# Kernel optimization log

Measured on AMD Instinct MI355X. Metric: run time of the kernel, lower is better.

Reference implementation:

```python
import jax, jax.numpy as jnp
import numpy as np

B, T, N, H, D = 8, 128, 170, 4, 16
F = H * D  # 64
LN_EPS = 1e-5
MASK_FILL = -(2.0 ** 15) + 1.0  # -32767, matches torch code


def setup_inputs() -> dict:
    key = jax.random.key(0)
    ks = jax.random.split(key, 16)
    s = 0.05
    def w(k):
        return jax.random.normal(k, (F, F), jnp.float32) * s
    def b(k):
        return jax.random.normal(k, (F,), jnp.float32) * s
    return {
        "x": jax.random.normal(ks[0], (B, T, N, F), jnp.float32),
        "te": jax.random.normal(ks[1], (B, T, N, F), jnp.float32),
        "Wq": w(ks[2]), "bq": b(ks[3]),
        "Wk": w(ks[4]), "bk": b(ks[5]),
        "Wv": w(ks[6]), "bv": b(ks[7]),
        "Wo": w(ks[8]), "bo": b(ks[9]),
        "Wf1": w(ks[10]), "bf1": b(ks[11]),
        "Wf2": w(ks[12]), "bf2": b(ks[13]),
    }


def _ln(v):
    # LayerNorm over last dim, elementwise_affine=False
    m = jnp.mean(v, axis=-1, keepdims=True)
    var = jnp.mean((v - m) ** 2, axis=-1, keepdims=True)
    return (v - m) / jnp.sqrt(var + LN_EPS)


def reference(x, te, Wq, bq, Wk, bk, Wv, bv, Wo, bo, Wf1, bf1, Wf2, bf2):
    x = x + te  # [B,T,N,F]
    # q/k/v projections (FeedForward with L=1 -> plain linear, no ReLU)
    q = (x @ Wq + bq).reshape(B, T, N, H, D)
    k = (x @ Wk + bk).reshape(B, T, N, H, D)
    v = (x @ Wv + bv).reshape(B, T, N, H, D)
    # attention over time axis, independent per node n and head h
    att = jnp.einsum('btnhd,bsnhd->bhnts', q, k) / jnp.sqrt(jnp.float32(D))
    causal = jnp.tril(jnp.ones((T, T), dtype=bool))  # keep s <= t
    att = jnp.where(causal[None, None, None, :, :], att, MASK_FILL)
    att = jax.nn.softmax(att, axis=-1)
    out = jnp.einsum('bhnts,bsnhd->btnhd', att, v).reshape(B, T, N, F)
    out = out @ Wo + bo  # ofc
    val = _ln(out + x)
    # ff: Linear-ReLU-Linear with residual + LN (res_ln=True)
    ff = jax.nn.relu(val @ Wf1 + bf1) @ Wf2 + bf2
    return _ln(ff + val)
```

## Files before the change

kernel.cpp:

```cpp
#include <hip/hip_runtime.h>

typedef __attribute__((ext_vector_type(8))) short short8;
typedef __attribute__((ext_vector_type(4))) float f32x4;
typedef __attribute__((ext_vector_type(16))) float f32x16;

#define B_ 8
#define T_ 128
#define N_ 170
#define F_ 64
#define ROWSTRIDE (N_ * F_)

__device__ __forceinline__ unsigned short f2bf(float f) {
    union { float f; unsigned u; } v; v.f = f;
    unsigned r = v.u + 0x7fffu + ((v.u >> 16) & 1u);
    return (unsigned short)(r >> 16);
}
__device__ __forceinline__ float bf2f(unsigned short b) {
    union { unsigned u; float f; } v; v.u = ((unsigned)b) << 16; return v.f;
}
__device__ __forceinline__ unsigned cvtpk(float lo, float hi) {
    unsigned d;
    asm("v_cvt_pk_bf16_f32 %0, %1, %2" : "=v"(d) : "v"(lo), "v"(hi));
    return d;
}
__device__ __forceinline__ void pl32(unsigned &a, unsigned &b) {
    asm("v_permlane32_swap_b32 %0, %1" : "+v"(a), "+v"(b));
}
__device__ __forceinline__ void pl16(unsigned &a, unsigned &b) {
    asm("v_permlane16_swap_b32 %0, %1" : "+v"(a), "+v"(b));
}
__device__ __forceinline__ int swz128(int row, int byteInRow) {
    return row * 128 + (byteInRow ^ ((row & 7) << 4));
}
__device__ __forceinline__ int swz256(int row, int byteInRow) {
    return row * 256 + (byteInRow ^ ((row & 15) << 4));
}
__device__ __forceinline__ short8 ldfrag16(const char* base, int row0, int kbyte, int lane) {
    int row = row0 + (lane & 15);
    return *(const short8*)(base + swz128(row, kbyte + ((lane >> 4) << 4)));
}
__device__ __forceinline__ short8 ldfrag16w(const char* base, int row0, int kbyte, int lane) {
    int row = row0 + (lane & 15);
    return *(const short8*)(base + swz256(row, kbyte + ((lane >> 4) << 4)));
}
__device__ __forceinline__ short8 ldfrag32(const char* base, int row0, int colbyte, int lane) {
    int row = row0 + (lane & 31);
    return *(const short8*)(base + swz128(row, colbyte + ((lane >> 5) << 4)));
}
__device__ __forceinline__ short8 wfragT(const unsigned short* __restrict__ wT, int nt, int kc, int lane) {
    int j  = nt * 16 + (lane & 15);
    int k0 = kc * 32 + ((lane >> 4) & 3) * 8;
    return *(const short8*)(wT + j * 64 + k0);
}
__device__ __forceinline__ f32x4 zero4() {
    f32x4 v = {0.f, 0.f, 0.f, 0.f};
    return v;
}
__device__ __forceinline__ f32x16 zero16() {
    f32x16 v = {0.f, 0.f, 0.f, 0.f, 0.f, 0.f, 0.f, 0.f,
                0.f, 0.f, 0.f, 0.f, 0.f, 0.f, 0.f, 0.f};
    return v;
}

__device__ __forceinline__ void ln64(const float (&z)[2][4][4], float (&o)[2][4][4]) {
#pragma unroll
    for (int mi = 0; mi < 2; ++mi)
#pragma unroll
    for (int r = 0; r < 4; ++r) {
        float s = z[mi][0][r] + z[mi][1][r] + z[mi][2][r] + z[mi][3][r];
        s += __shfl_xor(s, 1); s += __shfl_xor(s, 2);
        s += __shfl_xor(s, 4); s += __shfl_xor(s, 8);
        float mean = s * 0.015625f;
        float d[4]; float q = 0.f;
#pragma unroll
        for (int nt = 0; nt < 4; ++nt) { d[nt] = z[mi][nt][r] - mean; q += d[nt] * d[nt]; }
        q += __shfl_xor(q, 1); q += __shfl_xor(q, 2);
        q += __shfl_xor(q, 4); q += __shfl_xor(q, 8);
        float rstd = __builtin_amdgcn_rsqf(q * 0.015625f + 1e-5f);
#pragma unroll
        for (int nt = 0; nt < 4; ++nt) o[mi][nt][r] = d[nt] * rstd;
    }
}

__global__ void prep_weights(const float* __restrict__ Wq, const float* __restrict__ Wk,
                             const float* __restrict__ Wv, const float* __restrict__ Wo,
                             const float* __restrict__ Wf1, const float* __restrict__ Wf2,
                             unsigned short* __restrict__ ws) {
    const float* Ws[6] = {Wq, Wk, Wv, Wo, Wf1, Wf2};
    const float* W = Ws[blockIdx.x];
    unsigned short* o = ws + blockIdx.x * 4096;
#pragma unroll
    for (int i = 0; i < 16; ++i) {
        int idx = i * 256 + threadIdx.x;
        int j = idx >> 6, k = idx & 63;
        o[idx] = f2bf(W[k * 64 + j]);
    }
}

__global__ __launch_bounds__(256, 2)
void ta_fused(const float* __restrict__ x, const float* __restrict__ te,
              const unsigned short* __restrict__ wT,
              const float* __restrict__ bq, const float* __restrict__ bk,
              const float* __restrict__ bv, const float* __restrict__ bo,
              const float* __restrict__ bf1, const float* __restrict__ bf2,
              float* __restrict__ out)
{
    __shared__ __align__(16) char sXb[16384];
    __shared__ __align__(16) char sQb[16384];
    __shared__ __align__(16) char sKb[16384];
    __shared__ __align__(16) char sVO[16384];

    const int tid  = threadIdx.x;
    const int lane = tid & 63;
    const int wv   = tid >> 6;
    const int bid  = blockIdx.x;
    const int b    = bid / N_;
    const int n    = bid - b * N_;
    const long long base = ((long long)b * T_ * N_ + n) * F_;

    {
        const int row = tid >> 1;
        const int hf  = tid & 1;
        const float* xr = x  + base + (long long)row * ROWSTRIDE + hf * 32;
        const float* tr = te + base + (long long)row * ROWSTRIDE + hf * 32;
#pragma unroll
        for (int i = 0; i < 8; ++i) {
            float4 a = ((const float4*)xr)[i];
            float4 c = ((const float4*)tr)[i];
            unsigned d0 = cvtpk(a.x + c.x, a.y + c.y);
            unsigned d1 = cvtpk(a.z + c.z, a.w + c.w);
            unsigned long long pk = (unsigned long long)d0 | ((unsigned long long)d1 << 32);
            *(unsigned long long*)(sXb + swz128(row, (hf * 32 + i * 4) * 2)) = pk;
        }
    }
    __syncthreads();

    const int t0w = wv * 32;
    const int lg4 = (lane >> 4) & 3;

    {
        short8 ax[2][2];
#pragma unroll
        for (int mi = 0; mi < 2; ++mi)
#pragma unroll
        for (int kc = 0; kc < 2; ++kc)
            ax[mi][kc] = ldfrag16(sXb, t0w + mi * 16, kc * 64, lane);

        const float* bp[3] = {bq, bk, bv};
#pragma unroll
        for (int w = 0; w < 3; ++w) {
            const unsigned short* wTp = wT + w * 4096;
            short8 bw[4][2]; float bias[4];
#pragma unroll
            for (int nt = 0; nt < 4; ++nt) {
                bw[nt][0] = wfragT(wTp, nt, 0, lane);
                bw[nt][1] = wfragT(wTp, nt, 1, lane);
                bias[nt]  = bp[w][nt * 16 + (lane & 15)];
            }
            f32x4 acc[2][4];
#pragma unroll
            for (int mi = 0; mi < 2; ++mi)
#pragma unroll
            for (int nt = 0; nt < 4; ++nt) acc[mi][nt] = zero4();
#pragma unroll
            for (int kc = 0; kc < 2; ++kc)
#pragma unroll
            for (int mi = 0; mi < 2; ++mi)
#pragma unroll
            for (int nt = 0; nt < 4; ++nt)
                acc[mi][nt] = __builtin_amdgcn_mfma_f32_16x16x32_bf16(ax[mi][kc], bw[nt][kc], acc[mi][nt], 0, 0, 0);

            if (w < 2) {
                char* dst = (w == 0) ? sQb : sKb;
#pragma unroll
                for (int mi = 0; mi < 2; ++mi)
#pragma unroll
                for (int nt = 0; nt < 4; ++nt)
#pragma unroll
                for (int r = 0; r < 4; ++r) {
                    int t = t0w + mi * 16 + lg4 * 4 + r;
                    int f = nt * 16 + (lane & 15);
                    *(unsigned short*)(dst + swz128(t, f * 2)) = f2bf(acc[mi][nt][r] + bias[nt]);
                }
            } else {
#pragma unroll
                for (int mi = 0; mi < 2; ++mi)
#pragma unroll
                for (int nt = 0; nt < 4; ++nt) {
                    int f  = nt * 16 + (lane & 15);
                    int tb = t0w + mi * 16 + lg4 * 4;
                    unsigned d0 = cvtpk(acc[mi][nt][0] + bias[nt], acc[mi][nt][1] + bias[nt]);
                    unsigned d1 = cvtpk(acc[mi][nt][2] + bias[nt], acc[mi][nt][3] + bias[nt]);
                    unsigned long long pk = (unsigned long long)d0 | ((unsigned long long)d1 << 32);
                    *(unsigned long long*)(sVO + swz256(f, tb * 2)) = pk;
                }
            }
        }
    }
    __syncthreads();

    {
        const int h    = wv;
        const int colb = h * 32;
        short8 vf[4], kfc[4];
#pragma unroll
        for (int sb = 0; sb < 4; ++sb) {
            vf[sb]  = ldfrag16w(sVO, h * 16, sb * 64, lane);
            kfc[sb] = ldfrag32(sKb, sb * 32, colb, lane);
        }
        __syncthreads();

        const int tcol = lane & 31;
        const int hi4  = (lane >> 5) * 4;
#pragma unroll
        for (int tb = 0; tb < 4; ++tb) {
            short8 qf = ldfrag32(sQb, tb * 32, colb, lane);
            f32x16 sacc[4];
#pragma unroll
            for (int sb = 0; sb <= tb; ++sb)
                sacc[sb] = __builtin_amdgcn_mfma_f32_32x32x16_bf16(kfc[sb], qf, zero16(), 0, 0, 0);
#pragma unroll
            for (int r = 0; r < 16; ++r) {
                int srow = (r & 3) + 8 * (r >> 2) + hi4;
                if (srow > tcol) sacc[tb][r] = -3.0e38f;
            }
            float m = -3.0e38f;
#pragma unroll
            for (int sb = 0; sb <= tb; ++sb)
#pragma unroll
                for (int r = 0; r < 16; ++r) m = fmaxf(m, sacc[sb][r]);
            m = fmaxf(m, __shfl_xor(m, 32));
            float sum = 0.f;
#pragma unroll
            for (int sb = 0; sb <= tb; ++sb)
#pragma unroll
                for (int r = 0; r < 16; ++r) {
                    float p = __expf((sacc[sb][r] - m) * 0.25f);
                    sacc[sb][r] = p; sum += p;
                }
            sum += __shfl_xor(sum, 32);
            float rs = __builtin_amdgcn_rcpf(sum);

            f32x4 oacc[2];
            oacc[0] = zero4(); oacc[1] = zero4();
#pragma unroll
            for (int sb = 0; sb <= tb; ++sb) {
                float ps[16];
#pragma unroll
                for (int r = 0; r < 16; ++r) ps[r] = sacc[sb][r] * rs;
                unsigned a0 = cvtpk(ps[0],  ps[1]);
                unsigned a1 = cvtpk(ps[4],  ps[5]);
                unsigned a2 = cvtpk(ps[8],  ps[9]);
                unsigned a3 = cvtpk(ps[12], ps[13]);
                unsigned b0 = cvtpk(ps[2],  ps[3]);
                unsigned b1 = cvtpk(ps[6],  ps[7]);
                unsigned b2 = cvtpk(ps[10], ps[11]);
                unsigned b3 = cvtpk(ps[14], ps[15]);
                pl32(a0, a2); pl32(a1, a3);
                pl16(a0, a1); pl16(a2, a3);
                pl32(b0, b2); pl32(b1, b3);
                pl16(b0, b1); pl16(b2, b3);
                union { unsigned u[4]; short8 s; } F0, F1;
                F0.u[0] = a0; F0.u[1] = b0; F0.u[2] = a2; F0.u[3] = b2;
                F1.u[0] = a1; F1.u[1] = b1; F1.u[2] = a3; F1.u[3] = b3;
                oacc[0] = __builtin_amdgcn_mfma_f32_16x16x32_bf16(F0.s, vf[sb], oacc[0], 0, 0, 0);
                oacc[1] = __builtin_amdgcn_mfma_f32_16x16x32_bf16(F1.s, vf[sb], oacc[1], 0, 0, 0);
            }
#pragma unroll
            for (int mi = 0; mi < 2; ++mi)
#pragma unroll
            for (int r = 0; r < 4; ++r) {
                int t = tb * 32 + mi * 16 + lg4 * 4 + r;
                int f = h * 16 + (lane & 15);
                *(unsigned short*)(sVO + swz128(t, f * 2)) = f2bf(oacc[mi][r]);
            }
        }
    }
    __syncthreads();

    float val[2][4][4];
    {
        short8 af[2][2];
#pragma unroll
        for (int mi = 0; mi < 2; ++mi)
#pragma unroll
        for (int kc = 0; kc < 2; ++kc) af[mi][kc] = ldfrag16(sVO, t0w + mi * 16, kc * 64, lane);
        const unsigned short* wTp = wT + 3 * 4096;
        short8 bwf[4][2]; float bias[4];
#pragma unroll
        for (int nt = 0; nt < 4; ++nt) {
            bwf[nt][0] = wfragT(wTp, nt, 0, lane);
            bwf[nt][1] = wfragT(wTp, nt, 1, lane);
            bias[nt]   = bo[nt * 16 + (lane & 15)];
        }
        f32x4 acc[2][4];
#pragma unroll
        for (int mi = 0; mi < 2; ++mi)
#pragma unroll
        for (int nt = 0; nt < 4; ++nt) acc[mi][nt] = zero4();
#pragma unroll
        for (int kc = 0; kc < 2; ++kc)
#pragma unroll
        for (int mi = 0; mi < 2; ++mi)
#pragma unroll
        for (int nt = 0; nt < 4; ++nt)
            acc[mi][nt] = __builtin_amdgcn_mfma_f32_16x16x32_bf16(af[mi][kc], bwf[nt][kc], acc[mi][nt], 0, 0, 0);
        float z[2][4][4];
#pragma unroll
        for (int mi = 0; mi < 2; ++mi)
#pragma unroll
        for (int nt = 0; nt < 4; ++nt)
#pragma unroll
        for (int r = 0; r < 4; ++r) {
            int t = t0w + mi * 16 + lg4 * 4 + r;
            int f = nt * 16 + (lane & 15);
            float xv = bf2f(*(const unsigned short*)(sXb + swz128(t, f * 2)));
            z[mi][nt][r] = acc[mi][nt][r] + bias[nt] + xv;
        }
        ln64(z, val);
#pragma unroll
        for (int mi = 0; mi < 2; ++mi)
#pragma unroll
        for (int nt = 0; nt < 4; ++nt)
#pragma unroll
        for (int r = 0; r < 4; ++r) {
            int t = t0w + mi * 16 + lg4 * 4 + r;
            int f = nt * 16 + (lane & 15);
            *(unsigned short*)(sQb + swz128(t, f * 2)) = f2bf(val[mi][nt][r]);
        }
    }

    {
        short8 af[2][2];
#pragma unroll
        for (int mi = 0; mi < 2; ++mi)
#pragma unroll
        for (int kc = 0; kc < 2; ++kc) af[mi][kc] = ldfrag16(sQb, t0w + mi * 16, kc * 64, lane);
        const unsigned short* wTp = wT + 4 * 4096;
        short8 bwf[4][2]; float bias[4];
#pragma unroll
        for (int nt = 0; nt < 4; ++nt) {
            bwf[nt][0] = wfragT(wTp, nt, 0, lane);
            bwf[nt][1] = wfragT(wTp, nt, 1, lane);
            bias[nt]   = bf1[nt * 16 + (lane & 15)];
        }
        f32x4 acc[2][4];
#pragma unroll
        for (int mi = 0; mi < 2; ++mi)
#pragma unroll
        for (int nt = 0; nt < 4; ++nt) acc[mi][nt] = zero4();
#pragma unroll
        for (int kc = 0; kc < 2; ++kc)
#pragma unroll
        for (int mi = 0; mi < 2; ++mi)
#pragma unroll
        for (int nt = 0; nt < 4; ++nt)
            acc[mi][nt] = __builtin_amdgcn_mfma_f32_16x16x32_bf16(af[mi][kc], bwf[nt][kc], acc[mi][nt], 0, 0, 0);
#pragma unroll
        for (int mi = 0; mi < 2; ++mi)
#pragma unroll
        for (int nt = 0; nt < 4; ++nt)
#pragma unroll
        for (int r = 0; r < 4; ++r) {
            int t = t0w + mi * 16 + lg4 * 4 + r;
            int f = nt * 16 + (lane & 15);
            *(unsigned short*)(sKb + swz128(t, f * 2)) = f2bf(fmaxf(acc[mi][nt][r] + bias[nt], 0.f));
        }
    }

    {
        short8 af[2][2];
#pragma unroll
        for (int mi = 0; mi < 2; ++mi)
#pragma unroll
        for (int kc = 0; kc < 2; ++kc) af[mi][kc] = ldfrag16(sKb, t0w + mi * 16, kc * 64, lane);
        const unsigned short* wTp = wT + 5 * 4096;
        short8 bwf[4][2]; float bias[4];
#pragma unroll
        for (int nt = 0; nt < 4; ++nt) {
            bwf[nt][0] = wfragT(wTp, nt, 0, lane);
            bwf[nt][1] = wfragT(wTp, nt, 1, lane);
            bias[nt]   = bf2[nt * 16 + (lane & 15)];
        }
        f32x4 acc[2][4];
#pragma unroll
        for (int mi = 0; mi < 2; ++mi)
#pragma unroll
        for (int nt = 0; nt < 4; ++nt) acc[mi][nt] = zero4();
#pragma unroll
        for (int kc = 0; kc < 2; ++kc)
#pragma unroll
        for (int mi = 0; mi < 2; ++mi)
#pragma unroll
        for (int nt = 0; nt < 4; ++nt)
            acc[mi][nt] = __builtin_amdgcn_mfma_f32_16x16x32_bf16(af[mi][kc], bwf[nt][kc], acc[mi][nt], 0, 0, 0);
        float z[2][4][4], res[2][4][4];
#pragma unroll
        for (int mi = 0; mi < 2; ++mi)
#pragma unroll
        for (int nt = 0; nt < 4; ++nt)
#pragma unroll
        for (int r = 0; r < 4; ++r)
            z[mi][nt][r] = acc[mi][nt][r] + bias[nt] + val[mi][nt][r];
        ln64(z, res);
#pragma unroll
        for (int mi = 0; mi < 2; ++mi)
#pragma unroll
        for (int nt = 0; nt < 4; ++nt)
#pragma unroll
        for (int r = 0; r < 4; ++r) {
            int t = t0w + mi * 16 + lg4 * 4 + r;
            int f = nt * 16 + (lane & 15);
            out[base + (long long)t * ROWSTRIDE + f] = res[mi][nt][r];
        }
    }
}

extern "C" void kernel_launch(void* const* d_in, const int* in_sizes, int n_in,
                              void* d_out, int out_size, void* d_ws, size_t ws_size,
                              hipStream_t stream) {
    const float* x   = (const float*)d_in[0];
    const float* te  = (const float*)d_in[1];
    const float* Wq  = (const float*)d_in[2];
    const float* bq  = (const float*)d_in[3];
    const float* Wk  = (const float*)d_in[4];
    const float* bk  = (const float*)d_in[5];
    const float* Wv  = (const float*)d_in[6];
    const float* bv  = (const float*)d_in[7];
    const float* Wo  = (const float*)d_in[8];
    const float* bo  = (const float*)d_in[9];
    const float* Wf1 = (const float*)d_in[10];
    const float* bf1 = (const float*)d_in[11];
    const float* Wf2 = (const float*)d_in[12];
    const float* bf2 = (const float*)d_in[13];
    unsigned short* wsT = (unsigned short*)d_ws;

    prep_weights<<<dim3(6), dim3(256), 0, stream>>>(Wq, Wk, Wv, Wo, Wf1, Wf2, wsT);
    ta_fused<<<dim3(B_ * N_), dim3(256), 0, stream>>>(
        x, te, wsT, bq, bk, bv, bo, bf1, bf2, (float*)d_out);
}
```

Before: 81.36 us.

## Double threads per block to 512 and split attention row tiles across wave pairs

Raises the block from 4 to 8 waves. Each wave now owns 16 time rows instead of 32 in the projection, output-projection and FFN stages. In attention, two waves share each head, and the causal query tiles are split so each wave gets one short and one long tile (0/3 vs 1/2). This is meant to raise parallelism and latency hiding per block while cutting per-thread registers, at the cost of more waves competing for LDS and the same shared-memory footprint.

```diff
diff --git a/kernel.cpp b/kernel.cpp
--- a/kernel.cpp
+++ b/kernel.cpp
@@ -23,12 +23,6 @@
     asm("v_cvt_pk_bf16_f32 %0, %1, %2" : "=v"(d) : "v"(lo), "v"(hi));
     return d;
 }
-__device__ __forceinline__ void pl32(unsigned &a, unsigned &b) {
-    asm("v_permlane32_swap_b32 %0, %1" : "+v"(a), "+v"(b));
-}
-__device__ __forceinline__ void pl16(unsigned &a, unsigned &b) {
-    asm("v_permlane16_swap_b32 %0, %1" : "+v"(a), "+v"(b));
-}
 __device__ __forceinline__ int swz128(int row, int byteInRow) {
     return row * 128 + (byteInRow ^ ((row & 7) << 4));
 }
@@ -62,23 +56,21 @@
     return v;
 }
 
-__device__ __forceinline__ void ln64(const float (&z)[2][4][4], float (&o)[2][4][4]) {
-#pragma unroll
-    for (int mi = 0; mi < 2; ++mi)
+__device__ __forceinline__ void ln1(float (&z)[4][4]) {
 #pragma unroll
     for (int r = 0; r < 4; ++r) {
-        float s = z[mi][0][r] + z[mi][1][r] + z[mi][2][r] + z[mi][3][r];
+        float s = z[0][r] + z[1][r] + z[2][r] + z[3][r];
         s += __shfl_xor(s, 1); s += __shfl_xor(s, 2);
         s += __shfl_xor(s, 4); s += __shfl_xor(s, 8);
         float mean = s * 0.015625f;
         float d[4]; float q = 0.f;
 #pragma unroll
-        for (int nt = 0; nt < 4; ++nt) { d[nt] = z[mi][nt][r] - mean; q += d[nt] * d[nt]; }
+        for (int nt = 0; nt < 4; ++nt) { d[nt] = z[nt][r] - mean; q += d[nt] * d[nt]; }
         q += __shfl_xor(q, 1); q += __shfl_xor(q, 2);
         q += __shfl_xor(q, 4); q += __shfl_xor(q, 8);
         float rstd = __builtin_amdgcn_rsqf(q * 0.015625f + 1e-5f);
 #pragma unroll
-        for (int nt = 0; nt < 4; ++nt) o[mi][nt][r] = d[nt] * rstd;
+        for (int nt = 0; nt < 4; ++nt) z[nt][r] = d[nt] * rstd;
     }
 }
 
@@ -97,7 +89,7 @@
     }
 }
 
-__global__ __launch_bounds__(256, 2)
+__global__ __launch_bounds__(512, 2)
 void ta_fused(const float* __restrict__ x, const float* __restrict__ te,
               const unsigned short* __restrict__ wT,
               const float* __restrict__ bq, const float* __restrict__ bk,
@@ -113,38 +105,36 @@
     const int tid  = threadIdx.x;
     const int lane = tid & 63;
     const int wv   = tid >> 6;
+    const int lam  = lane & 15;
+    const int g    = (lane >> 4) & 3;
     const int bid  = blockIdx.x;
     const int b    = bid / N_;
     const int n    = bid - b * N_;
     const long long base = ((long long)b * T_ * N_ + n) * F_;
-
-    {
-        const int row = tid >> 1;
-        const int hf  = tid & 1;
-        const float* xr = x  + base + (long long)row * ROWSTRIDE + hf * 32;
-        const float* tr = te + base + (long long)row * ROWSTRIDE + hf * 32;
-#pragma unroll
-        for (int i = 0; i < 8; ++i) {
+    const int t0w = wv * 16;
+
+    {
+        const int row = tid >> 2;
+        const int seg = tid & 3;
+        const float* xr = x  + base + (long long)row * ROWSTRIDE + seg * 16;
+        const float* tr = te + base + (long long)row * ROWSTRIDE + seg * 16;
+#pragma unroll
+        for (int i = 0; i < 4; ++i) {
             float4 a = ((const float4*)xr)[i];
             float4 c = ((const float4*)tr)[i];
             unsigned d0 = cvtpk(a.x + c.x, a.y + c.y);
             unsigned d1 = cvtpk(a.z + c.z, a.w + c.w);
             unsigned long long pk = (unsigned long long)d0 | ((unsigned long long)d1 << 32);
-            *(unsigned long long*)(sXb + swz128(row, (hf * 32 + i * 4) * 2)) = pk;
+            *(unsigned long long*)(sXb + swz128(row, (seg * 16 + i * 4) * 2)) = pk;
         }
     }
     __syncthreads();
 
-    const int t0w = wv * 32;
-    const int lg4 = (lane >> 4) & 3;
-
-    {
-        short8 ax[2][2];
-#pragma unroll
-        for (int mi = 0; mi < 2; ++mi)
+    {
+        short8 ax[2];
 #pragma unroll
         for (int kc = 0; kc < 2; ++kc)
-            ax[mi][kc] = ldfrag16(sXb, t0w + mi * 16, kc * 64, lane);
+            ax[kc] = ldfrag16(sXb, t0w, kc * 64, lane);
 
         const float* bp[3] = {bq, bk, bv};
 #pragma unroll
@@ -155,44 +145,36 @@
             for (int nt = 0; nt < 4; ++nt) {
                 bw[nt][0] = wfragT(wTp, nt, 0, lane);
                 bw[nt][1] = wfragT(wTp, nt, 1, lane);
-                bias[nt]  = bp[w][nt * 16 + (lane & 15)];
+                bias[nt]  = bp[w][nt * 16 + lam];
             }
-            f32x4 acc[2][4];
-#pragma unroll
-            for (int mi = 0; mi < 2; ++mi)
-#pragma unroll
-            for (int nt = 0; nt < 4; ++nt) acc[mi][nt] = zero4();
+            f32x4 acc[4];
+#pragma unroll
+            for (int nt = 0; nt < 4; ++nt) acc[nt] = zero4();
 #pragma unroll
             for (int kc = 0; kc < 2; ++kc)
 #pragma unroll
-            for (int mi = 0; mi < 2; ++mi)
-#pragma unroll
             for (int nt = 0; nt < 4; ++nt)
-                acc[mi][nt] = __builtin_amdgcn_mfma_f32_16x16x32_bf16(ax[mi][kc], bw[nt][kc], acc[mi][nt], 0, 0, 0);
+                acc[nt] = __builtin_amdgcn_mfma_f32_16x16x32_bf16(ax[kc], bw[nt][kc], acc[nt], 0, 0, 0);
 
             if (w < 2) {
                 char* dst = (w == 0) ? sQb : sKb;
 #pragma unroll
-                for (int mi = 0; mi < 2; ++mi)
-#pragma unroll
                 for (int nt = 0; nt < 4; ++nt)
 #pragma unroll
                 for (int r = 0; r < 4; ++r) {
-                    int t = t0w + mi * 16 + lg4 * 4 + r;
-                    int f = nt * 16 + (lane & 15);
-                    *(unsigned short*)(dst + swz128(t, f * 2)) = f2bf(acc[mi][nt][r] + bias[nt]);
+                    int t = t0w + g * 4 + r;
+                    int f = nt * 16 + lam;
+                    *(unsigned short*)(dst + swz128(t, f * 2)) = f2bf(acc[nt][r] + bias[nt]);
                 }
             } else {
 #pragma unroll
-                for (int mi = 0; mi < 2; ++mi)
-#pragma unroll
                 for (int nt = 0; nt < 4; ++nt) {
-                    int f  = nt * 16 + (lane & 15);
-                    int tb = t0w + mi * 16 + lg4 * 4;
-                    unsigned d0 = cvtpk(acc[mi][nt][0] + bias[nt], acc[mi][nt][1] + bias[nt]);
-                    unsigned d1 = cvtpk(acc[mi][nt][2] + bias[nt], acc[mi][nt][3] + bias[nt]);
-                    unsigned long long pk = (unsigned long long)d0 | ((unsigned long long)d1 << 32);
-                    *(unsigned long long*)(sVO + swz256(f, tb * 2)) = pk;
+                    int f   = nt * 16 + lam;
+                    int tb0 = t0w + g * 4;
+                    unsigned d0 = cvtpk(acc[nt][0] + bias[nt], acc[nt][1] + bias[nt]);
+                    unsigned d1 = cvtpk(acc[nt][2] + bias[nt], acc[nt][3] + bias[nt]);
+                    unsigned long long pkv = (unsigned long long)d0 | ((unsigned long long)d1 << 32);
+                    *(unsigned long long*)(sVO + swz256(f, tb0 * 2)) = pkv;
                 }
             }
         }
@@ -200,7 +182,8 @@
     __syncthreads();
 
     {
-        const int h    = wv;
+        const int h    = wv >> 1;
+        const int th   = wv & 1;
         const int colb = h * 32;
         short8 vf[4], kfc[4];
 #pragma unroll
@@ -214,6 +197,7 @@
         const int hi4  = (lane >> 5) * 4;
 #pragma unroll
         for (int tb = 0; tb < 4; ++tb) {
+            if (((tb == 0 || tb == 3) ? 0 : 1) != th) continue;
             short8 qf = ldfrag32(sQb, tb * 32, colb, lane);
             f32x16 sacc[4];
 #pragma unroll
@@ -256,10 +240,14 @@
                 unsigned b1 = cvtpk(ps[6],  ps[7]);
                 unsigned b2 = cvtpk(ps[10], ps[11]);
                 unsigned b3 = cvtpk(ps[14], ps[15]);
-                pl32(a0, a2); pl32(a1, a3);
-                pl16(a0, a1); pl16(a2, a3);
-                pl32(b0, b2); pl32(b1, b3);
-                pl16(b0, b1); pl16(b2, b3);
+                asm("v_permlane32_swap_b32 %0, %1" : "+v"(a0), "+v"(a2));
+                asm("v_permlane32_swap_b32 %0, %1" : "+v"(a1), "+v"(a3));
+                asm("v_permlane16_swap_b32 %0, %1" : "+v"(a0), "+v"(a1));
+                asm("v_permlane16_swap_b32 %0, %1" : "+v"(a2), "+v"(a3));
+                asm("v_permlane32_swap_b32 %0, %1" : "+v"(b0), "+v"(b2));
+                asm("v_permlane32_swap_b32 %0, %1" : "+v"(b1), "+v"(b3));
+                asm("v_permlane16_swap_b32 %0, %1" : "+v"(b0), "+v"(b1));
+                asm("v_permlane16_swap_b32 %0, %1" : "+v"(b2), "+v"(b3));
                 union { unsigned u[4]; short8 s; } F0, F1;
                 F0.u[0] = a0; F0.u[1] = b0; F0.u[2] = a2; F0.u[3] = b2;
                 F1.u[0] = a1; F1.u[1] = b1; F1.u[2] = a3; F1.u[3] = b3;
@@ -270,148 +258,119 @@
             for (int mi = 0; mi < 2; ++mi)
 #pragma unroll
             for (int r = 0; r < 4; ++r) {
-                int t = tb * 32 + mi * 16 + lg4 * 4 + r;
-                int f = h * 16 + (lane & 15);
+                int t = tb * 32 + mi * 16 + g * 4 + r;
+                int f = h * 16 + lam;
                 *(unsigned short*)(sVO + swz128(t, f * 2)) = f2bf(oacc[mi][r]);
             }
         }
     }
     __syncthreads();
 
-    float val[2][4][4];
-    {
-        short8 af[2][2];
-#pragma unroll
-        for (int mi = 0; mi < 2; ++mi)
-#pragma unroll
-        for (int kc = 0; kc < 2; ++kc) af[mi][kc] = ldfrag16(sVO, t0w + mi * 16, kc * 64, lane);
+    float val[4][4];
+    {
+        short8 af[2];
+#pragma unroll
+        for (int kc = 0; kc < 2; ++kc) af[kc] = ldfrag16(sVO, t0w, kc * 64, lane);
         const unsigned short* wTp = wT + 3 * 4096;
         short8 bwf[4][2]; float bias[4];
 #pragma unroll
         for (int nt = 0; nt < 4; ++nt) {
             bwf[nt][0] = wfragT(wTp, nt, 0, lane);
             bwf[nt][1] = wfragT(wTp, nt, 1, lane);
-            bias[nt]   = bo[nt * 16 + (lane & 15)];
-        }
-        f32x4 acc[2][4];
-#pragma unroll
-        for (int mi = 0; mi < 2; ++mi)
-#pragma unroll
-        for (int nt = 0; nt < 4; ++nt) acc[mi][nt] = zero4();
+            bias[nt]   = bo[nt * 16 + lam];
+        }
+        f32x4 acc[4];
+#pragma unroll
+        for (int nt = 0; nt < 4; ++nt) acc[nt] = zero4();
 #pragma unroll
         for (int kc = 0; kc < 2; ++kc)
 #pragma unroll
-        for (int mi = 0; mi < 2; ++mi)
-#pragma unroll
-        for (int nt = 0; nt < 4; ++nt)
-            acc[mi][nt] = __builtin_amdgcn_mfma_f32_16x16x32_bf16(af[mi][kc], bwf[nt][kc], acc[mi][nt], 0, 0, 0);
-        float z[2][4][4];
-#pragma unroll
-        for (int mi = 0; mi < 2; ++mi)
+        for (int nt = 0; nt < 4; ++nt)
+            acc[nt] = __builtin_amdgcn_mfma_f32_16x16x32_bf16(af[kc], bwf[nt][kc], acc[nt], 0, 0, 0);
 #pragma unroll
         for (int nt = 0; nt < 4; ++nt)
 #pragma unroll
         for (int r = 0; r < 4; ++r) {
-            int t = t0w + mi * 16 + lg4 * 4 + r;
-            int f = nt * 16 + (lane & 15);
+            int t = t0w + g * 4 + r;
+            int f = nt * 16 + lam;
             float xv = bf2f(*(const unsigned short*)(sXb + swz128(t, f * 2)));
-            z[mi][nt][r] = acc[mi][nt][r] + bias[nt] + xv;
-        }
-        ln64(z, val);
-#pragma unroll
-        for (int mi = 0; mi < 2; ++mi)
+            val[nt][r] = acc[nt][r] + bias[nt] + xv;
+        }
+        ln1(val);
 #pragma unroll
         for (int nt = 0; nt < 4; ++nt)
 #pragma unroll
         for (int r = 0; r < 4; ++r) {
-            int t = t0w + mi * 16 + lg4 * 4 + r;
-            int f = nt * 16 + (lane & 15);
-            *(unsigned short*)(sQb + swz128(t, f * 2)) = f2bf(val[mi][nt][r]);
-        }
-    }
-
-    {
-        short8 af[2][2];
-#pragma unroll
-        for (int mi = 0; mi < 2; ++mi)
-#pragma unroll
-        for (int kc = 0; kc < 2; ++kc) af[mi][kc] = ldfrag16(sQb, t0w + mi * 16, kc * 64, lane);
+            int t = t0w + g * 4 + r;
+            int f = nt * 16 + lam;
+            *(unsigned short*)(sQb + swz128(t, f * 2)) = f2bf(val[nt][r]);
+        }
+    }
+
+    {
+        short8 af[2];
+#pragma unroll
+        for (int kc = 0; kc < 2; ++kc) af[kc] = ldfrag16(sQb, t0w, kc * 64, lane);
         const unsigned short* wTp = wT + 4 * 4096;
         short8 bwf[4][2]; float bias[4];
 #pragma unroll
         for (int nt = 0; nt < 4; ++nt) {
             bwf[nt][0] = wfragT(wTp, nt, 0, lane);
             bwf[nt][1] = wfragT(wTp, nt, 1, lane);
-            bias[nt]   = bf1[nt * 16 + (lane & 15)];
-        }
-        f32x4 acc[2][4];
-#pragma unroll
-        for (int mi = 0; mi < 2; ++mi)
-#pragma unroll
-        for (int nt = 0; nt < 4; ++nt) acc[mi][nt] = zero4();
+            bias[nt]   = bf1[nt * 16 + lam];
+        }
+        f32x4 acc[4];
+#pragma unroll
+        for (int nt = 0; nt < 4; ++nt) acc[nt] = zero4();
 #pragma unroll
         for (int kc = 0; kc < 2; ++kc)
 #pragma unroll
-        for (int mi = 0; mi < 2; ++mi)
-#pragma unroll
-        for (int nt = 0; nt < 4; ++nt)
-            acc[mi][nt] = __builtin_amdgcn_mfma_f32_16x16x32_bf16(af[mi][kc], bwf[nt][kc], acc[mi][nt], 0, 0, 0);
-#pragma unroll
-        for (int mi = 0; mi < 2; ++mi)
+        for (int nt = 0; nt < 4; ++nt)
+            acc[nt] = __builtin_amdgcn_mfma_f32_16x16x32_bf16(af[kc], bwf[nt][kc], acc[nt], 0, 0, 0);
 #pragma unroll
         for (int nt = 0; nt < 4; ++nt)
 #pragma unroll
         for (int r = 0; r < 4; ++r) {
-            int t = t0w + mi * 16 + lg4 * 4 + r;
-            int f = nt * 16 + (lane & 15);
-            *(unsigned short*)(sKb + swz128(t, f * 2)) = f2bf(fmaxf(acc[mi][nt][r] + bias[nt], 0.f));
-        }
-    }
-
-    {
-        short8 af[2][2];
-#pragma unroll
-        for (int mi = 0; mi < 2; ++mi)
-#pragma unroll
-        for (int kc = 0; kc < 2; ++kc) af[mi][kc] = ldfrag16(sKb, t0w + mi * 16, kc * 64, lane);
+            int t = t0w + g * 4 + r;
+            int f = nt * 16 + lam;
+            *(unsigned short*)(sKb + swz128(t, f * 2)) = f2bf(fmaxf(acc[nt][r] + bias[nt], 0.f));
+        }
+    }
+
+    {
+        short8 af[2];
+#pragma unroll
+        for (int kc = 0; kc < 2; ++kc) af[kc] = ldfrag16(sKb, t0w, kc * 64, lane);
         const unsigned short* wTp = wT + 5 * 4096;
         short8 bwf[4][2]; float bias[4];
 #pragma unroll
         for (int nt = 0; nt < 4; ++nt) {
             bwf[nt][0] = wfragT(wTp, nt, 0, lane);
             bwf[nt][1] = wfragT(wTp, nt, 1, lane);
-            bias[nt]   = bf2[nt * 16 + (lane & 15)];
-        }
-        f32x4 acc[2][4];
-#pragma unroll
-        for (int mi = 0; mi < 2; ++mi)
-#pragma unroll
-        for (int nt = 0; nt < 4; ++nt) acc[mi][nt] = zero4();
+            bias[nt]   = bf2[nt * 16 + lam];
+        }
+        f32x4 acc[4];
+#pragma unroll
+        for (int nt = 0; nt < 4; ++nt) acc[nt] = zero4();
 #pragma unroll
         for (int kc = 0; kc < 2; ++kc)
 #pragma unroll
-        for (int mi = 0; mi < 2; ++mi)
-#pragma unroll
-        for (int nt = 0; nt < 4; ++nt)
-            acc[mi][nt] = __builtin_amdgcn_mfma_f32_16x16x32_bf16(af[mi][kc], bwf[nt][kc], acc[mi][nt], 0, 0, 0);
-        float z[2][4][4], res[2][4][4];
-#pragma unroll
-        for (int mi = 0; mi < 2; ++mi)
+        for (int nt = 0; nt < 4; ++nt)
+            acc[nt] = __builtin_amdgcn_mfma_f32_16x16x32_bf16(af[kc], bwf[nt][kc], acc[nt], 0, 0, 0);
+        float z[4][4];
 #pragma unroll
         for (int nt = 0; nt < 4; ++nt)
 #pragma unroll
         for (int r = 0; r < 4; ++r)
-            z[mi][nt][r] = acc[mi][nt][r] + bias[nt] + val[mi][nt][r];
-        ln64(z, res);
-#pragma unroll
-        for (int mi = 0; mi < 2; ++mi)
+            z[nt][r] = acc[nt][r] + bias[nt] + val[nt][r];
+        ln1(z);
 #pragma unroll
         for (int nt = 0; nt < 4; ++nt)
 #pragma unroll
         for (int r = 0; r < 4; ++r) {
-            int t = t0w + mi * 16 + lg4 * 4 + r;
-            int f = nt * 16 + (lane & 15);
-            out[base + (long long)t * ROWSTRIDE + f] = res[mi][nt][r];
+            int t = t0w + g * 4 + r;
+            int f = nt * 16 + lam;
+            out[base + (long long)t * ROWSTRIDE + f] = z[nt][r];
         }
     }
 }
@@ -436,6 +395,6 @@
     unsigned short* wsT = (unsigned short*)d_ws;
 
     prep_weights<<<dim3(6), dim3(256), 0, stream>>>(Wq, Wk, Wv, Wo, Wf1, Wf2, wsT);
-    ta_fused<<<dim3(B_ * N_), dim3(256), 0, stream>>>(
+    ta_fused<<<dim3(B_ * N_), dim3(512), 0, stream>>>(
         x, te, wsT, bq, bk, bv, bo, bf1, bf2, (float*)d_out);
 }
```

Result: slower. 119.6 us (+47.0%).

## Load x+te straight into MFMA fragments, drop staging LDS buffer, raise occupancy

Applied to the files above, without the earlier changes.

Each wave now reads x and te from global memory directly into its bf16 MFMA A-fragments and keeps an fp32 copy of x+te in registers for the residual, so the 16KB sXb shared buffer and its barrier go away. The residual before the first LayerNorm now uses full fp32 x+te rather than a bf16-rounded copy. With 48KB of LDS per block, launch bounds ask for 3 blocks per SM to raise occupancy. In exchange, x and te are read from global memory twice with less coalesced per-element residual loads, and register pressure rises, which could cause spills under the tighter launch bound.

```diff
diff --git a/kernel.cpp b/kernel.cpp
--- a/kernel.cpp
+++ b/kernel.cpp
@@ -10,24 +10,17 @@
 #define F_ 64
 #define ROWSTRIDE (N_ * F_)
 
+union U4 { unsigned u[4]; short8 s; };
+
 __device__ __forceinline__ unsigned short f2bf(float f) {
     union { float f; unsigned u; } v; v.f = f;
     unsigned r = v.u + 0x7fffu + ((v.u >> 16) & 1u);
     return (unsigned short)(r >> 16);
 }
-__device__ __forceinline__ float bf2f(unsigned short b) {
-    union { unsigned u; float f; } v; v.u = ((unsigned)b) << 16; return v.f;
-}
 __device__ __forceinline__ unsigned cvtpk(float lo, float hi) {
     unsigned d;
     asm("v_cvt_pk_bf16_f32 %0, %1, %2" : "=v"(d) : "v"(lo), "v"(hi));
     return d;
-}
-__device__ __forceinline__ void pl32(unsigned &a, unsigned &b) {
-    asm("v_permlane32_swap_b32 %0, %1" : "+v"(a), "+v"(b));
-}
-__device__ __forceinline__ void pl16(unsigned &a, unsigned &b) {
-    asm("v_permlane16_swap_b32 %0, %1" : "+v"(a), "+v"(b));
 }
 __device__ __forceinline__ int swz128(int row, int byteInRow) {
     return row * 128 + (byteInRow ^ ((row & 7) << 4));
@@ -97,7 +90,7 @@
     }
 }
 
-__global__ __launch_bounds__(256, 2)
+__global__ __launch_bounds__(256, 3)
 void ta_fused(const float* __restrict__ x, const float* __restrict__ te,
               const unsigned short* __restrict__ wT,
               const float* __restrict__ bq, const float* __restrict__ bk,
@@ -105,7 +98,6 @@
               const float* __restrict__ bf1, const float* __restrict__ bf2,
               float* __restrict__ out)
 {
-    __shared__ __align__(16) char sXb[16384];
     __shared__ __align__(16) char sQb[16384];
     __shared__ __align__(16) char sKb[16384];
     __shared__ __align__(16) char sVO[16384];
@@ -113,39 +105,45 @@
     const int tid  = threadIdx.x;
     const int lane = tid & 63;
     const int wv   = tid >> 6;
+    const int lam  = lane & 15;
+    const int g    = (lane >> 4) & 3;
     const int bid  = blockIdx.x;
     const int b    = bid / N_;
     const int n    = bid - b * N_;
     const long long base = ((long long)b * T_ * N_ + n) * F_;
+    const int t0w = wv * 32;
+    const int lg4 = g;
+
+    short8 ax[2][2];
+    float xres[2][4][4];
+#pragma unroll
+    for (int mi = 0; mi < 2; ++mi) {
+        const float* xr = x  + base + (long long)(t0w + mi * 16 + lam) * ROWSTRIDE;
+        const float* tr = te + base + (long long)(t0w + mi * 16 + lam) * ROWSTRIDE;
+#pragma unroll
+        for (int kc = 0; kc < 2; ++kc) {
+            int f0 = kc * 32 + g * 8;
+            float4 a0 = *(const float4*)(xr + f0);
+            float4 a1 = *(const float4*)(xr + f0 + 4);
+            float4 c0 = *(const float4*)(tr + f0);
+            float4 c1 = *(const float4*)(tr + f0 + 4);
+            U4 u;
+            u.u[0] = cvtpk(a0.x + c0.x, a0.y + c0.y);
+            u.u[1] = cvtpk(a0.z + c0.z, a0.w + c0.w);
+            u.u[2] = cvtpk(a1.x + c1.x, a1.y + c1.y);
+            u.u[3] = cvtpk(a1.z + c1.z, a1.w + c1.w);
+            ax[mi][kc] = u.s;
+        }
+#pragma unroll
+        for (int nt = 0; nt < 4; ++nt)
+#pragma unroll
+        for (int r = 0; r < 4; ++r) {
+            long long off = base + (long long)(t0w + mi * 16 + g * 4 + r) * ROWSTRIDE + nt * 16 + lam;
+            xres[mi][nt][r] = x[off] + te[off];
+        }
+    }
 
     {
-        const int row = tid >> 1;
-        const int hf  = tid & 1;
-        const float* xr = x  + base + (long long)row * ROWSTRIDE + hf * 32;
-        const float* tr = te + base + (long long)row * ROWSTRIDE + hf * 32;
-#pragma unroll
-        for (int i = 0; i < 8; ++i) {
-            float4 a = ((const float4*)xr)[i];
-            float4 c = ((const float4*)tr)[i];
-            unsigned d0 = cvtpk(a.x + c.x, a.y + c.y);
-            unsigned d1 = cvtpk(a.z + c.z, a.w + c.w);
-            unsigned long long pk = (unsigned long long)d0 | ((unsigned long long)d1 << 32);
-            *(unsigned long long*)(sXb + swz128(row, (hf * 32 + i * 4) * 2)) = pk;
-        }
-    }
-    __syncthreads();
-
-    const int t0w = wv * 32;
-    const int lg4 = (lane >> 4) & 3;
-
-    {
-        short8 ax[2][2];
-#pragma unroll
-        for (int mi = 0; mi < 2; ++mi)
-#pragma unroll
-        for (int kc = 0; kc < 2; ++kc)
-            ax[mi][kc] = ldfrag16(sXb, t0w + mi * 16, kc * 64, lane);
-
         const float* bp[3] = {bq, bk, bv};
 #pragma unroll
         for (int w = 0; w < 3; ++w) {
@@ -155,7 +153,7 @@
             for (int nt = 0; nt < 4; ++nt) {
                 bw[nt][0] = wfragT(wTp, nt, 0, lane);
                 bw[nt][1] = wfragT(wTp, nt, 1, lane);
-                bias[nt]  = bp[w][nt * 16 + (lane & 15)];
+                bias[nt]  = bp[w][nt * 16 + lam];
             }
             f32x4 acc[2][4];
 #pragma unroll
@@ -179,7 +177,7 @@
 #pragma unroll
                 for (int r = 0; r < 4; ++r) {
                     int t = t0w + mi * 16 + lg4 * 4 + r;
-                    int f = nt * 16 + (lane & 15);
+                    int f = nt * 16 + lam;
                     *(unsigned short*)(dst + swz128(t, f * 2)) = f2bf(acc[mi][nt][r] + bias[nt]);
                 }
             } else {
@@ -187,12 +185,12 @@
                 for (int mi = 0; mi < 2; ++mi)
 #pragma unroll
                 for (int nt = 0; nt < 4; ++nt) {
-                    int f  = nt * 16 + (lane & 15);
-                    int tb = t0w + mi * 16 + lg4 * 4;
+                    int f   = nt * 16 + lam;
+                    int tb0 = t0w + mi * 16 + lg4 * 4;
                     unsigned d0 = cvtpk(acc[mi][nt][0] + bias[nt], acc[mi][nt][1] + bias[nt]);
                     unsigned d1 = cvtpk(acc[mi][nt][2] + bias[nt], acc[mi][nt][3] + bias[nt]);
-                    unsigned long long pk = (unsigned long long)d0 | ((unsigned long long)d1 << 32);
-                    *(unsigned long long*)(sVO + swz256(f, tb * 2)) = pk;
+                    unsigned long long pkv = (unsigned long long)d0 | ((unsigned long long)d1 << 32);
+                    *(unsigned long long*)(sVO + swz256(f, tb0 * 2)) = pkv;
                 }
             }
         }
@@ -256,11 +254,15 @@
                 unsigned b1 = cvtpk(ps[6],  ps[7]);
                 unsigned b2 = cvtpk(ps[10], ps[11]);
                 unsigned b3 = cvtpk(ps[14], ps[15]);
-                pl32(a0, a2); pl32(a1, a3);
-                pl16(a0, a1); pl16(a2, a3);
-                pl32(b0, b2); pl32(b1, b3);
-                pl16(b0, b1); pl16(b2, b3);
-                union { unsigned u[4]; short8 s; } F0, F1;
+                asm("v_permlane32_swap_b32 %0, %1" : "+v"(a0), "+v"(a2));
+                asm("v_permlane32_swap_b32 %0, %1" : "+v"(a1), "+v"(a3));
+                asm("v_permlane16_swap_b32 %0, %1" : "+v"(a0), "+v"(a1));
+                asm("v_permlane16_swap_b32 %0, %1" : "+v"(a2), "+v"(a3));
+                asm("v_permlane32_swap_b32 %0, %1" : "+v"(b0), "+v"(b2));
+                asm("v_permlane32_swap_b32 %0, %1" : "+v"(b1), "+v"(b3));
+                asm("v_permlane16_swap_b32 %0, %1" : "+v"(b0), "+v"(b1));
+                asm("v_permlane16_swap_b32 %0, %1" : "+v"(b2), "+v"(b3));
+                U4 F0, F1;
                 F0.u[0] = a0; F0.u[1] = b0; F0.u[2] = a2; F0.u[3] = b2;
                 F1.u[0] = a1; F1.u[1] = b1; F1.u[2] = a3; F1.u[3] = b3;
                 oacc[0] = __builtin_amdgcn_mfma_f32_16x16x32_bf16(F0.s, vf[sb], oacc[0], 0, 0, 0);
@@ -271,7 +273,7 @@
 #pragma unroll
             for (int r = 0; r < 4; ++r) {
                 int t = tb * 32 + mi * 16 + lg4 * 4 + r;
-                int f = h * 16 + (lane & 15);
+                int f = h * 16 + lam;
                 *(unsigned short*)(sVO + swz128(t, f * 2)) = f2bf(oacc[mi][r]);
             }
         }
@@ -291,7 +293,7 @@
         for (int nt = 0; nt < 4; ++nt) {
             bwf[nt][0] = wfragT(wTp, nt, 0, lane);
             bwf[nt][1] = wfragT(wTp, nt, 1, lane);
-            bias[nt]   = bo[nt * 16 + (lane & 15)];
+            bias[nt]   = bo[nt * 16 + lam];
         }
         f32x4 acc[2][4];
 #pragma unroll
@@ -311,21 +313,17 @@
 #pragma unroll
         for (int nt = 0; nt < 4; ++nt)
 #pragma unroll
+        for (int r = 0; r < 4; ++r)
+            z[mi][nt][r] = acc[mi][nt][r] + bias[nt] + xres[mi][nt][r];
+        ln64(z, val);
+#pragma unroll
+        for (int mi = 0; mi < 2; ++mi)
+#pragma unroll
+        for (int nt = 0; nt < 4; ++nt)
+#pragma unroll
         for (int r = 0; r < 4; ++r) {
             int t = t0w + mi * 16 + lg4 * 4 + r;
-            int f = nt * 16 + (lane & 15);
-            float xv = bf2f(*(const unsigned short*)(sXb + swz128(t, f * 2)));
-            z[mi][nt][r] = acc[mi][nt][r] + bias[nt] + xv;
-        }
-        ln64(z, val);
-#pragma unroll
-        for (int mi = 0; mi < 2; ++mi)
-#pragma unroll
-        for (int nt = 0; nt < 4; ++nt)
-#pragma unroll
-        for (int r = 0; r < 4; ++r) {
-            int t = t0w + mi * 16 + lg4 * 4 + r;
-            int f = nt * 16 + (lane & 15);
+            int f = nt * 16 + lam;
             *(unsigned short*)(sQb + swz128(t, f * 2)) = f2bf(val[mi][nt][r]);
         }
     }
@@ -342,7 +340,7 @@
         for (int nt = 0; nt < 4; ++nt) {
             bwf[nt][0] = wfragT(wTp, nt, 0, lane);
             bwf[nt][1] = wfragT(wTp, nt, 1, lane);
-            bias[nt]   = bf1[nt * 16 + (lane & 15)];
+            bias[nt]   = bf1[nt * 16 + lam];
         }
         f32x4 acc[2][4];
 #pragma unroll
@@ -363,7 +361,7 @@
 #pragma unroll
         for (int r = 0; r < 4; ++r) {
             int t = t0w + mi * 16 + lg4 * 4 + r;
-            int f = nt * 16 + (lane & 15);
+            int f = nt * 16 + lam;
             *(unsigned short*)(sKb + swz128(t, f * 2)) = f2bf(fmaxf(acc[mi][nt][r] + bias[nt], 0.f));
         }
     }
@@ -380,7 +378,7 @@
         for (int nt = 0; nt < 4; ++nt) {
             bwf[nt][0] = wfragT(wTp, nt, 0, lane);
             bwf[nt][1] = wfragT(wTp, nt, 1, lane);
-            bias[nt]   = bf2[nt * 16 + (lane & 15)];
+            bias[nt]   = bf2[nt * 16 + lam];
         }
         f32x4 acc[2][4];
 #pragma unroll
@@ -410,7 +408,7 @@
 #pragma unroll
         for (int r = 0; r < 4; ++r) {
             int t = t0w + mi * 16 + lg4 * 4 + r;
-            int f = nt * 16 + (lane & 15);
+            int f = nt * 16 + lam;
             out[base + (long long)t * ROWSTRIDE + f] = res[mi][nt][r];
         }
     }
```

Result: slower. 124.5 us (+53.0%).
